# Performance work log

Measured on AMD Instinct MI355X. Metric: run time of the kernel, lower is better.

The kernel has to match this reference:

```python
import jax, jax.numpy as jnp
import numpy as np

T, N = 20, 192
D_EMB, D_H, D_REL = 32, 64, 32
D_TMP = D_REL + 2 * D_H  # 160 = rel_emb + h_self + h_neighbor


def setup_inputs() -> dict:
    key = jax.random.key(0)
    ks = jax.random.split(key, 16)
    g = lambda i, shape, s: jax.random.normal(ks[i], shape, jnp.float32) * s
    inp = {
        "nodes_abs": g(0, (T, N, 2), 1.0),
        "nodes_norm": g(1, (T, N, 2), 1.0),
        "shift_value": g(2, (T, N, 2), 1.0),
        # parameters (inputLayer, LSTMCell, 2 GCNs, outputLayer)
        "w_in": g(3, (D_EMB, 2), 0.2),
        "b_in": jnp.zeros((D_EMB,), jnp.float32),
        "w_ih": g(4, (4 * D_H, D_EMB), 0.1),
        "w_hh": g(5, (4 * D_H, D_H), 0.001),
        "b_ih": jnp.zeros((4 * D_H,), jnp.float32).at[D_H:2 * D_H].set(1.0),
        "b_hh": jnp.zeros((4 * D_H,), jnp.float32),
        "w_rel": g(6, (2, D_REL, 2), 0.1),
        "b_rel": jnp.zeros((2, D_REL), jnp.float32),
        "w_gate": g(7, (2, D_H, D_TMP), 0.1),
        "b_gate": jnp.zeros((2, D_H), jnp.float32),
        "w_ar": g(8, (2, D_TMP), 0.1),
        "b_ar": jnp.zeros((2,), jnp.float32),
        "w_nei": g(9, (2, D_H, D_H), 0.1),
        "w_out": g(10, (2, D_H), 0.1),
        "b_out": jnp.zeros((2,), jnp.float32),
        # int inputs
        "seq_list": jax.random.randint(ks[11], (T, N), 0, 2).astype(jnp.int32),
        "nei_list": jax.random.randint(ks[12], (T, N, N), 0, 2).astype(jnp.int32),
        "nei_num": jax.random.randint(ks[13], (T, N), 0, N).astype(jnp.int32),
    }
    return inp


def reference(nodes_abs, nodes_norm, shift_value, w_in, b_in, w_ih, w_hh, b_ih, b_hh,
              w_rel, b_rel, w_gate, b_gate, w_ar, b_ar, w_nei, w_out, b_out,
              seq_list, nei_list, nei_num):
    eps = 1e-6

    def gcn(p, corr, nei_f, h, c, o):
        # corr: (N,N,2) relative positions pos_i - pos_j; nei_f: (N,N) 0/1 mask
        r = jax.nn.relu(jnp.einsum('ijd,rd->ijr', corr, w_rel[p]) + b_rel[p])
        tmp = jnp.concatenate([r,
                               jnp.broadcast_to(h[:, None, :], (N, N, D_H)),
                               jnp.broadcast_to(h[None, :, :], (N, N, D_H))], axis=-1)
        gate = jax.nn.sigmoid(jnp.einsum('ijt,ht->ijh', tmp, w_gate[p]) + b_gate[p])
        score = jnp.einsum('ijt,t->ij', tmp, w_ar[p]) + b_ar[p]
        score = jnp.where(nei_f > 0, score, -1e9)
        pos = jax.nn.softmax(score, axis=1) * nei_f  # masked attention over neighbors j
        msg = jnp.einsum('ij,ijh,jh->ih', pos, gate, h)  # gated, attended aggregation
        c_new = c + msg @ w_nei[p].T
        h_new = o * jnp.tanh(c_new)
        v1 = jnp.sum(gate * nei_f[:, :, None]) / (jnp.sum(nei_f) * D_H + eps)
        v2 = jnp.sum(jnp.max(pos, axis=1)) / (jnp.sum(jnp.max(nei_f, axis=1)) + eps)
        v3 = jnp.sum(nei_f) / jnp.float32(N)
        return h_new, c_new, (v1, v2, v3)

    def step(carry, xs):
        h, c, v1s, v2s, v3s = carry
        abs_t, norm_t, seq_t, nei_t = xs
        m = seq_t > 0
        mf = m.astype(jnp.float32)
        nei_f = (nei_t > 0).astype(jnp.float32) * mf[:, None] * mf[None, :]
        corr = abs_t[:, None, :] - abs_t[None, :, :]  # corr_index[i,j] = pos_i - pos_j
        x = jax.nn.relu(norm_t @ w_in.T + b_in)  # dropout is identity in eval
        gates = x @ w_ih.T + b_ih + h @ w_hh.T + b_hh
        i_g, f_g, g_g, o_g = jnp.split(gates, 4, axis=-1)
        i_g = jax.nn.sigmoid(i_g); f_g = jax.nn.sigmoid(f_g); o_g = jax.nn.sigmoid(o_g)
        c1 = f_g * c + i_g * jnp.tanh(g_g)
        h1 = o_g * jnp.tanh(c1)
        h1, c1, look = gcn(0, corr, nei_f, h1, c1, o_g)
        h1, c1, _ = gcn(1, corr, nei_f, h1, c1, o_g)
        out_t = (h1 @ w_out.T + b_out) * mf[:, None]
        h = jnp.where(m[:, None], h1, h)  # only active nodes update state
        c = jnp.where(m[:, None], c1, c)
        return (h, c, v1s + look[0], v2s + look[1], v3s + look[2]), out_t

    h0 = jnp.zeros((N, D_H), jnp.float32)
    c0 = jnp.zeros((N, D_H), jnp.float32)
    z = jnp.float32(0.0)
    xs = (nodes_abs[:-1], nodes_norm[:-1], seq_list[:-1], nei_list[:-1])
    (h, c, v1, v2, v3), outs = jax.lax.scan(step, (h0, c0, z, z, z), xs)
    outputs = jnp.concatenate([outs, jnp.zeros((1, N, 2), jnp.float32)], axis=0)
    return outputs, h, c, (v1 / T, v2 / T, v3 / T)
```

## Files before the change

kernel.cpp:

```cpp
#include <hip/hip_runtime.h>
#include <hip/hip_bf16.h>

#define T_STEPS 20
#define NSTEP   19
#define NN      192
#define DH      64
#define DE      32

enum : int {
  O_H     = 0,
  O_C     = O_H    + NN*DH,
  O_UH0   = O_C    + NN*DH,
  O_UH1   = O_UH0  + 2*NN*DH,
  O_CW    = O_UH1  + 2*NN*DH,
  O_OG    = O_CW   + NN*DH,
  O_U1    = O_OG   + NN*DH,
  O_S1    = O_U1   + NN*DH,
  O_S20   = O_S1   + NN,
  O_S21   = O_S20  + NN,
  O_ACC   = O_S21  + NN,
  O_WIHT  = O_ACC  + NSTEP*4 + 4,
  O_WHHT  = O_WIHT + 8192,
  O_BIH   = O_WHHT + 16384,
  O_WIN   = O_BIH  + 256,
  O_BIN   = O_WIN  + 64,
  O_WRELF = O_BIN  + 32,
  O_BRELF = O_WRELF+ 128,
  O_WGR   = O_BRELF+ 64,
  O_WGH1T = O_WGR  + 4096,
  O_WGH2T = O_WGH1T+ 8192,
  O_BGATE = O_WGH2T+ 8192,
  O_WARR  = O_BGATE+ 128,
  O_WARH1 = O_WARR + 64,
  O_WARH2 = O_WARH1+ 128,
  O_BAR   = O_WARH2+ 128,
  O_WNEIT = O_BAR  + 4,
  O_WOUT  = O_WNEIT+ 8192,
  O_BOUT  = O_WOUT + 128,
  O_ISF   = O_BOUT + 2,
  O_TOTAL = O_ISF  + 1
};

typedef unsigned long long ull;

__device__ __forceinline__ float bf2f(__hip_bfloat16 v) { return __bfloat162float(v); }
__device__ __forceinline__ float sigm(float x) { return 1.0f / (1.0f + __expf(-x)); }
__device__ __forceinline__ float tanh_fast(float x) {
  float e = __expf(-2.0f * fabsf(x));
  float r = (1.0f - e) / (1.0f + e);
  return copysignf(r, x);
}

__device__ __forceinline__ float ldf(const void* p, int idx, int isf32) {
  if (isf32) return ((const float*)p)[idx];
  return bf2f(((const __hip_bfloat16*)p)[idx]);
}
__device__ __forceinline__ void stf(void* p, int idx, float v, int isf32) {
  if (isf32) ((float*)p)[idx] = v;
  else       ((__hip_bfloat16*)p)[idx] = __float2bfloat16(v);
}

__device__ __forceinline__ int read_isf(const float* F, int tid, int* s_isf) {
  if (tid == 0) *s_isf = (int)F[O_ISF];
  __syncthreads();
  return *s_isf;
}

__device__ __forceinline__ void lstm_prep_dev(
    float* __restrict__ F, const void* __restrict__ nnorm, int isf32,
    int t, int i, int tid, int wave, int lane, int load_hc,
    float* s_x, float* s_hc, float* s_cc, float* s_gates, float* s_h1)
{
  if (load_hc && wave == 0) { s_hc[lane] = F[O_H + i*DH + lane]; s_cc[lane] = F[O_C + i*DH + lane]; }
  if (wave == 1 && lane < DE) {
    float nx = ldf(nnorm, (t*NN + i)*2 + 0, isf32);
    float ny = ldf(nnorm, (t*NN + i)*2 + 1, isf32);
    s_x[lane] = fmaxf(nx*F[O_WIN + lane*2] + ny*F[O_WIN + lane*2 + 1] + F[O_BIN + lane], 0.f);
  }
  __syncthreads();
  {
    int G = tid;
    float acc = F[O_BIH + G];
    for (int e = 0; e < DE; e++) acc += F[O_WIHT + e*256 + G] * s_x[e];
    for (int k = 0; k < DH; k++) acc += F[O_WHHT + k*256 + G] * s_hc[k];
    s_gates[G] = acc;
  }
  __syncthreads();
  if (wave == 0) {
    float ig = sigm(s_gates[lane]);
    float fg = sigm(s_gates[64 + lane]);
    float gg = tanh_fast(s_gates[128 + lane]);
    float og = sigm(s_gates[192 + lane]);
    float c1 = fg * s_cc[lane] + ig * gg;
    float h1 = og * tanh_fast(c1);
    int idx = i*DH + lane;
    F[O_CW  + idx] = c1;
    F[O_UH0 + 2*idx + 1] = h1;
    F[O_OG  + idx] = og;
    s_h1[lane] = h1;
  }
  __syncthreads();
  {
    int idx = i*DH + lane;
    if (wave == 0) {
      float a = 0.f;
      const float* w = F + O_WGH1T + lane;
      for (int k = 0; k < DH; k++) a += w[k*DH] * s_h1[k];
      F[O_U1 + idx] = a;
    } else if (wave == 1) {
      float a = 0.f;
      const float* w = F + O_WGH2T + lane;
      for (int k = 0; k < DH; k++) a += w[k*DH] * s_h1[k];
      F[O_UH0 + 2*idx] = a;
    } else if (wave == 2) {
      float hp = s_h1[lane];
      float a1 = hp * F[O_WARH1 + lane];
      float a2 = hp * F[O_WARH2 + lane];
      for (int o = 32; o >= 1; o >>= 1) { a1 += __shfl_xor(a1, o, 64); a2 += __shfl_xor(a2, o, 64); }
      if (lane == 0) { F[O_S1 + i] = a1; F[O_S20 + i] = a2; }
    }
  }
}

__global__ __launch_bounds__(256) void k_init(float* __restrict__ F,
                       void* __restrict__ out,
                       const void* w_in,  const void* b_in,
                       const void* w_ih,  const void* w_hh,
                       const void* b_ih,  const void* b_hh,
                       const void* w_rel, const void* b_rel,
                       const void* w_gate,const void* b_gate,
                       const void* w_ar,  const void* b_ar,
                       const void* w_nei, const void* w_out,
                       const void* b_out) {
  __shared__ int s_isf;
  const int wave = threadIdx.x >> 6, lane = threadIdx.x & 63;
  if (wave == 0) {
    const unsigned short* u = (const unsigned short*)w_gate;
    int bad = 0;
    for (int x = lane; x < 1024; x += 64) {
      float v = __uint_as_float(((unsigned)u[x]) << 16);
      if (!(fabsf(v) <= 4.0f)) bad++;
    }
    for (int o = 32; o >= 1; o >>= 1) bad += __shfl_xor(bad, o, 64);
    if (lane == 0) s_isf = (bad > 64);
  }
  __syncthreads();
  const int isf32 = s_isf;
  if (blockIdx.x == 0 && threadIdx.x == 0) F[O_ISF] = (float)isf32;

  int tid = blockIdx.x * blockDim.x + threadIdx.x;
  int stride = gridDim.x * blockDim.x;
  for (int x = tid; x < O_WIHT; x += stride) F[x] = 0.f;
  for (int x = tid; x < NN*2;  x += stride) stf(out, (T_STEPS-1)*NN*2 + x, 0.f, isf32);
  for (int x = tid; x < 8192;  x += stride) { int e = x >> 8, G = x & 255; F[O_WIHT + x] = ldf(w_ih, G*32 + e, isf32); }
  for (int x = tid; x < 16384; x += stride) { int k = x >> 8, G = x & 255; F[O_WHHT + x] = ldf(w_hh, G*64 + k, isf32); }
  for (int x = tid; x < 256;   x += stride) F[O_BIH + x] = ldf(b_ih, x, isf32) + ldf(b_hh, x, isf32);
  for (int x = tid; x < 64;    x += stride) F[O_WIN + x] = ldf(w_in, x, isf32);
  for (int x = tid; x < 32;    x += stride) F[O_BIN + x] = ldf(b_in, x, isf32);
  for (int x = tid; x < 128;   x += stride) F[O_WRELF + x] = ldf(w_rel, x, isf32);
  for (int x = tid; x < 64;    x += stride) F[O_BRELF + x] = ldf(b_rel, x, isf32);
  for (int x = tid; x < 4096;  x += stride) { int p = x >> 11, h = (x >> 5) & 63, d = x & 31;
    F[O_WGR + x] = ldf(w_gate, p*10240 + h*160 + d, isf32); }
  for (int x = tid; x < 8192;  x += stride) { int p = x >> 12, k = (x >> 6) & 63, h = x & 63;
    F[O_WGH1T + x] = ldf(w_gate, p*10240 + h*160 + 32 + k, isf32); }
  for (int x = tid; x < 8192;  x += stride) { int p = x >> 12, k = (x >> 6) & 63, h = x & 63;
    F[O_WGH2T + x] = ldf(w_gate, p*10240 + h*160 + 96 + k, isf32); }
  for (int x = tid; x < 128;   x += stride) F[O_BGATE + x] = ldf(b_gate, x, isf32);
  for (int x = tid; x < 64;    x += stride) { int p = x >> 5, d = x & 31; F[O_WARR + x] = ldf(w_ar, p*160 + d, isf32); }
  for (int x = tid; x < 128;   x += stride) { int p = x >> 6, k = x & 63; F[O_WARH1 + x] = ldf(w_ar, p*160 + 32 + k, isf32); }
  for (int x = tid; x < 128;   x += stride) { int p = x >> 6, k = x & 63; F[O_WARH2 + x] = ldf(w_ar, p*160 + 96 + k, isf32); }
  for (int x = tid; x < 2;     x += stride) F[O_BAR + x] = ldf(b_ar, x, isf32);
  for (int x = tid; x < 8192;  x += stride) { int p = x >> 12, k = (x >> 6) & 63, h = x & 63;
    F[O_WNEIT + x] = ldf(w_nei, p*4096 + h*64 + k, isf32); }
  for (int x = tid; x < 128;   x += stride) F[O_WOUT + x] = ldf(w_out, x, isf32);
  for (int x = tid; x < 2;     x += stride) F[O_BOUT + x] = ldf(b_out, x, isf32);
}

__global__ __launch_bounds__(256) void k_lstm0(float* __restrict__ F,
                                               const void* __restrict__ nnorm) {
  __shared__ float s_x[DE], s_hc[DH], s_cc[DH], s_gates[4*DH], s_h1[DH];
  __shared__ int s_isf;
  const int tid = threadIdx.x, wave = tid >> 6, lane = tid & 63;
  const int isf32 = read_isf(F, tid, &s_isf);
  lstm_prep_dev(F, nnorm, isf32, 0, blockIdx.x, tid, wave, lane, 1,
                s_x, s_hc, s_cc, s_gates, s_h1);
}

__global__ __launch_bounds__(256) void k_gcn(float* __restrict__ F,
                                             const void* __restrict__ nabs,
                                             const void* __restrict__ nnorm,
                                             const int* __restrict__ seq,
                                             const int* __restrict__ nei,
                                             void* __restrict__ out,
                                             int t, int p, int last) {
  __shared__ float s_rt[NN*33];
  __shared__ float s_score[NN], s_pos[NN], s_neif[NN];
  __shared__ int   s_jlist[NN];
  __shared__ float s_red[4*DH], s_v1[4], s_msg[DH], s_hprep[DH];
  __shared__ float s_x[DE], s_hc[DH], s_cc[DH], s_gates[4*DH], s_h1[DH];
  __shared__ int   s_isf, s_nv;

  const int tid = threadIdx.x, wave = tid >> 6, lane = tid & 63;
  const int i = blockIdx.x;
  const int isf32 = read_isf(F, tid, &s_isf);
  const int m_i = seq[t*NN + i] > 0;
  const int UHr = p ? O_UH1 : O_UH0;
  const int S2r = p ? O_S21 : O_S20;

  if (wave < 3) {
    int j  = wave*64 + lane;
    int nf = m_i && (seq[t*NN + j] > 0) && (nei[(t*NN + i)*NN + j] > 0);
    s_neif[j] = nf ? 1.f : 0.f;
    float sc = 0.f;
    if (nf) {
      float cx = ldf(nabs, (t*NN + i)*2 + 0, isf32) - ldf(nabs, (t*NN + j)*2 + 0, isf32);
      float cy = ldf(nabs, (t*NN + i)*2 + 1, isf32) - ldf(nabs, (t*NN + j)*2 + 1, isf32);
      const float* wr = F + O_WRELF + p*64;
      const float* br = F + O_BRELF + p*32;
      const float* wa = F + O_WARR  + p*32;
      float dot = 0.f;
      for (int d = 0; d < 32; d++) {
        float rv = fmaxf(cx*wr[2*d] + cy*wr[2*d+1] + br[d], 0.f);
        s_rt[j*33 + d] = rv;
        dot += rv * wa[d];
      }
      sc = dot + F[O_S1 + i] + F[S2r + j] + F[O_BAR + p];
    }
    s_score[j] = sc;
  }
  __syncthreads();

  if (wave == 0) {
    float n0 = s_neif[lane], n1 = s_neif[64+lane], n2 = s_neif[128+lane];
    float sc0 = s_score[lane], sc1 = s_score[64+lane], sc2 = s_score[128+lane];
    const float NEG = -3.0e38f;
    float mx = fmaxf(fmaxf(n0 > 0.f ? sc0 : NEG, n1 > 0.f ? sc1 : NEG),
                     n2 > 0.f ? sc2 : NEG);
    for (int o = 32; o >= 1; o >>= 1) mx = fmaxf(mx, __shfl_xor(mx, o, 64));
    float e0 = (n0 > 0.f) ? __expf(sc0 - mx) : 0.f;
    float e1 = (n1 > 0.f) ? __expf(sc1 - mx) : 0.f;
    float e2 = (n2 > 0.f) ? __expf(sc2 - mx) : 0.f;
    float s = e0 + e1 + e2;
    for (int o = 32; o >= 1; o >>= 1) s += __shfl_xor(s, o, 64);
    float inv = (s > 0.f) ? 1.0f / s : 0.f;
    float p0 = e0*inv, p1 = e1*inv, p2 = e2*inv;
    s_pos[lane] = p0; s_pos[64+lane] = p1; s_pos[128+lane] = p2;
    ull m0 = __ballot(n0 > 0.f), m1 = __ballot(n1 > 0.f), m2 = __ballot(n2 > 0.f);
    ull lt = (1ull << lane) - 1ull;
    int c0 = __popcll(m0), c1 = __popcll(m1);
    if (n0 > 0.f) s_jlist[__popcll(m0 & lt)] = lane;
    if (n1 > 0.f) s_jlist[c0 + __popcll(m1 & lt)] = 64 + lane;
    if (n2 > 0.f) s_jlist[c0 + c1 + __popcll(m2 & lt)] = 128 + lane;
    if (lane == 0) s_nv = c0 + c1 + __popcll(m2);
    if (p == 0 && m_i) {
      float cnt = n0 + n1 + n2;
      float pm  = fmaxf(fmaxf(p0, p1), p2);
      for (int o = 32; o >= 1; o >>= 1) {
        cnt += __shfl_xor(cnt, o, 64);
        pm   = fmaxf(pm, __shfl_xor(pm, o, 64));
      }
      if (lane == 0 && cnt > 0.f) {
        atomicAdd(&F[O_ACC + t*4 + 1], cnt);
        atomicAdd(&F[O_ACC + t*4 + 2], pm);
        atomicAdd(&F[O_ACC + t*4 + 3], 1.f);
      }
    }
  }
  __syncthreads();

  {
    float msg = 0.f, v1 = 0.f;
    const int nv = s_nv;
    if (m_i && nv > 0) {
      float wreg[32];
      const float* wgp = F + O_WGR + p*2048 + lane*32;
#pragma unroll
      for (int d = 0; d < 32; d++) wreg[d] = wgp[d];
      float basev = F[O_U1 + i*DH + lane] + F[O_BGATE + p*DH + lane];
      const float2* UH2 = (const float2*)(F + UHr);
      int k = wave;
      int jn = (k < nv) ? s_jlist[k] : 0;
      float2 uhn = (k < nv) ? UH2[jn*DH + lane] : make_float2(0.f, 0.f);
      for (; k < nv; k += 4) {
        int j = jn;
        float2 uh = uhn;
        int kn = k + 4;
        if (kn < nv) { jn = s_jlist[kn]; uhn = UH2[jn*DH + lane]; }
        float acc = basev + uh.x;
        const float* rr = &s_rt[j*33];
#pragma unroll
        for (int d = 0; d < 32; d++) acc += rr[d] * wreg[d];
        float g = sigm(acc);
        v1 += g;
        msg += s_pos[j] * g * uh.y;
      }
    }
    s_red[wave*DH + lane] = msg;
    for (int o = 32; o >= 1; o >>= 1) v1 += __shfl_xor(v1, o, 64);
    if (lane == 0) s_v1[wave] = v1;
  }
  __syncthreads();

  if (wave == 0) {
    s_msg[lane] = s_red[lane] + s_red[64+lane] + s_red[128+lane] + s_red[192+lane];
    if (p == 0 && m_i && lane == 0) {
      float v1t = s_v1[0] + s_v1[1] + s_v1[2] + s_v1[3];
      atomicAdd(&F[O_ACC + t*4 + 0], v1t);
    }
  }
  __syncthreads();

  if (wave == 0) {
    int idx = i*DH + lane;
    float hcom, ccom = 0.f;
    if (m_i) {
      float cn = F[O_CW + idx];
      const float* wn = F + O_WNEIT + p*4096 + lane;
      for (int k = 0; k < DH; k++) cn += s_msg[k] * wn[k*DH];
      hcom = F[O_OG + idx] * tanh_fast(cn);
      F[O_CW + idx] = cn;
      ccom = cn;
      if (p == 1) { F[O_H + idx] = hcom; F[O_C + idx] = ccom; }
    } else {
      hcom = F[UHr + 2*idx + 1];
    }
    if (p == 0) F[O_UH1 + 2*idx + 1] = hcom;
    s_hprep[lane] = hcom;
    if (p == 1) {
      s_hc[lane] = m_i ? hcom : F[O_H + idx];
      s_cc[lane] = m_i ? ccom : F[O_C + idx];
    }
  }
  __syncthreads();

  if (p == 0) {
    int idx = i*DH + lane;
    if (wave == 0) {
      float a = 0.f;
      const float* w = F + O_WGH1T + 4096 + lane;
      for (int k = 0; k < DH; k++) a += w[k*DH] * s_hprep[k];
      F[O_U1 + idx] = a;
    } else if (wave == 1) {
      float a = 0.f;
      const float* w = F + O_WGH2T + 4096 + lane;
      for (int k = 0; k < DH; k++) a += w[k*DH] * s_hprep[k];
      F[O_UH1 + 2*idx] = a;
    } else if (wave == 2) {
      float hp = s_hprep[lane];
      float a1 = hp * F[O_WARH1 + DH + lane];
      float a2 = hp * F[O_WARH2 + DH + lane];
      for (int o = 32; o >= 1; o >>= 1) { a1 += __shfl_xor(a1, o, 64); a2 += __shfl_xor(a2, o, 64); }
      if (lane == 0) { F[O_S1 + i] = a1; F[O_S21 + i] = a2; }
    }
  } else {
    if (wave == 0 && lane < 2) {
      float a = 0.f;
      if (m_i) {
        a = F[O_BOUT + lane];
        const float* wo = F + O_WOUT + lane*DH;
        for (int h = 0; h < DH; h++) a += s_hprep[h] * wo[h];
      }
      stf(out, (t*NN + i)*2 + lane, a, isf32);
    }
    if (!last) {
      lstm_prep_dev(F, nnorm, isf32, t + 1, i, tid, wave, lane, 0,
                    s_x, s_hc, s_cc, s_gates, s_h1);
    } else {
      if (wave == 0) stf(out, T_STEPS*NN*2 + i*DH + lane,         s_hc[lane], isf32);
      if (wave == 1) stf(out, T_STEPS*NN*2 + NN*DH + i*DH + lane, s_cc[lane], isf32);
      if (i == 0 && tid == 0) {
        float v1 = 0.f, v2 = 0.f, v3 = 0.f;
        for (int tt = 0; tt < NSTEP; tt++) {
          float sg = F[O_ACC + tt*4 + 0], sn = F[O_ACC + tt*4 + 1];
          float sp = F[O_ACC + tt*4 + 2], sm = F[O_ACC + tt*4 + 3];
          v1 += sg / (sn * 64.f + 1e-6f);
          v2 += sp / (sm + 1e-6f);
          v3 += sn / 192.f;
        }
        int base = T_STEPS*NN*2 + 2*NN*DH;
        stf(out, base + 0, v1 / 20.f, isf32);
        stf(out, base + 1, v2 / 20.f, isf32);
        stf(out, base + 2, v3 / 20.f, isf32);
      }
    }
  }
}

extern "C" void kernel_launch(void* const* d_in, const int* in_sizes, int n_in,
                              void* d_out, int out_size, void* d_ws, size_t ws_size,
                              hipStream_t stream) {
  const void* nabs  = d_in[0];
  const void* nnorm = d_in[1];
  const int* seq = (const int*)d_in[18];
  const int* nei = (const int*)d_in[19];
  float* F = (float*)d_ws;

  k_init<<<NN, 256, 0, stream>>>(F, d_out,
      d_in[3], d_in[4], d_in[5], d_in[6], d_in[7], d_in[8], d_in[9], d_in[10],
      d_in[11], d_in[12], d_in[13], d_in[14], d_in[15], d_in[16], d_in[17]);
  k_lstm0<<<NN, 256, 0, stream>>>(F, nnorm);
  for (int t = 0; t < NSTEP; t++) {
    k_gcn<<<NN, 256, 0, stream>>>(F, nabs, nnorm, seq, nei, d_out, t, 0, 0);
    k_gcn<<<NN, 256, 0, stream>>>(F, nabs, nnorm, seq, nei, d_out, t, 1, t == NSTEP - 1);
  }
}
```

Baseline: 650.7 us.

## Fuse all timesteps into one persistent kernel with grid barriers and on-chip state

Replaces the 38 per-step GCN kernel launches and the separate LSTM kernel with a single persistent kernel of 192 blocks. The blocks synchronise through a software grid barrier built on global atomics. Per-node LSTM and cell state (c, o-gate, u1, s1, h, c) now stays in shared memory across steps instead of going through global memory. Weights are loaded once into registers and LDS, and the gate-weight layout is transposed for that preload. This removes launch overhead and repeated weight reloads. The cost is a spin barrier that relies on all 192 blocks being co-resident, plus higher register and LDS pressure.

```diff
diff --git a/kernel.cpp b/kernel.cpp
--- a/kernel.cpp
+++ b/kernel.cpp
@@ -8,18 +8,13 @@
 #define DE      32
 
 enum : int {
-  O_H     = 0,
-  O_C     = O_H    + NN*DH,
-  O_UH0   = O_C    + NN*DH,
+  O_UH0   = 0,
   O_UH1   = O_UH0  + 2*NN*DH,
-  O_CW    = O_UH1  + 2*NN*DH,
-  O_OG    = O_CW   + NN*DH,
-  O_U1    = O_OG   + NN*DH,
-  O_S1    = O_U1   + NN*DH,
-  O_S20   = O_S1   + NN,
+  O_S20   = O_UH1  + 2*NN*DH,
   O_S21   = O_S20  + NN,
   O_ACC   = O_S21  + NN,
-  O_WIHT  = O_ACC  + NSTEP*4 + 4,
+  O_GBAR  = O_ACC  + NSTEP*4,
+  O_WIHT  = O_GBAR + 4,
   O_WHHT  = O_WIHT + 8192,
   O_BIH   = O_WHHT + 16384,
   O_WIN   = O_BIH  + 256,
@@ -66,60 +61,24 @@
   return *s_isf;
 }
 
-__device__ __forceinline__ void lstm_prep_dev(
-    float* __restrict__ F, const void* __restrict__ nnorm, int isf32,
-    int t, int i, int tid, int wave, int lane, int load_hc,
-    float* s_x, float* s_hc, float* s_cc, float* s_gates, float* s_h1)
-{
-  if (load_hc && wave == 0) { s_hc[lane] = F[O_H + i*DH + lane]; s_cc[lane] = F[O_C + i*DH + lane]; }
-  if (wave == 1 && lane < DE) {
-    float nx = ldf(nnorm, (t*NN + i)*2 + 0, isf32);
-    float ny = ldf(nnorm, (t*NN + i)*2 + 1, isf32);
-    s_x[lane] = fmaxf(nx*F[O_WIN + lane*2] + ny*F[O_WIN + lane*2 + 1] + F[O_BIN + lane], 0.f);
-  }
-  __syncthreads();
-  {
-    int G = tid;
-    float acc = F[O_BIH + G];
-    for (int e = 0; e < DE; e++) acc += F[O_WIHT + e*256 + G] * s_x[e];
-    for (int k = 0; k < DH; k++) acc += F[O_WHHT + k*256 + G] * s_hc[k];
-    s_gates[G] = acc;
-  }
-  __syncthreads();
-  if (wave == 0) {
-    float ig = sigm(s_gates[lane]);
-    float fg = sigm(s_gates[64 + lane]);
-    float gg = tanh_fast(s_gates[128 + lane]);
-    float og = sigm(s_gates[192 + lane]);
-    float c1 = fg * s_cc[lane] + ig * gg;
-    float h1 = og * tanh_fast(c1);
-    int idx = i*DH + lane;
-    F[O_CW  + idx] = c1;
-    F[O_UH0 + 2*idx + 1] = h1;
-    F[O_OG  + idx] = og;
-    s_h1[lane] = h1;
-  }
-  __syncthreads();
-  {
-    int idx = i*DH + lane;
-    if (wave == 0) {
-      float a = 0.f;
-      const float* w = F + O_WGH1T + lane;
-      for (int k = 0; k < DH; k++) a += w[k*DH] * s_h1[k];
-      F[O_U1 + idx] = a;
-    } else if (wave == 1) {
-      float a = 0.f;
-      const float* w = F + O_WGH2T + lane;
-      for (int k = 0; k < DH; k++) a += w[k*DH] * s_h1[k];
-      F[O_UH0 + 2*idx] = a;
-    } else if (wave == 2) {
-      float hp = s_h1[lane];
-      float a1 = hp * F[O_WARH1 + lane];
-      float a2 = hp * F[O_WARH2 + lane];
-      for (int o = 32; o >= 1; o >>= 1) { a1 += __shfl_xor(a1, o, 64); a2 += __shfl_xor(a2, o, 64); }
-      if (lane == 0) { F[O_S1 + i] = a1; F[O_S20 + i] = a2; }
-    }
-  }
+__device__ __forceinline__ void gridbar(float* F, unsigned ep) {
+  __syncthreads();
+  if (threadIdx.x == 0) {
+    __threadfence();
+    unsigned* bar = (unsigned*)(F + O_GBAR);
+    unsigned v = __hip_atomic_fetch_add(bar, 1u, __ATOMIC_RELAXED,
+                                        __HIP_MEMORY_SCOPE_AGENT) + 1u;
+    if (v == (ep + 1u) * (unsigned)NN) {
+      __hip_atomic_store(bar + 1, ep + 1u, __ATOMIC_RELEASE,
+                         __HIP_MEMORY_SCOPE_AGENT);
+    } else {
+      while (__hip_atomic_load(bar + 1, __ATOMIC_RELAXED,
+                               __HIP_MEMORY_SCOPE_AGENT) < ep + 1u)
+        __builtin_amdgcn_s_sleep(2);
+    }
+    __threadfence();
+  }
+  __syncthreads();
 }
 
 __global__ __launch_bounds__(256) void k_init(float* __restrict__ F,
@@ -159,7 +118,7 @@
   for (int x = tid; x < 32;    x += stride) F[O_BIN + x] = ldf(b_in, x, isf32);
   for (int x = tid; x < 128;   x += stride) F[O_WRELF + x] = ldf(w_rel, x, isf32);
   for (int x = tid; x < 64;    x += stride) F[O_BRELF + x] = ldf(b_rel, x, isf32);
-  for (int x = tid; x < 4096;  x += stride) { int p = x >> 11, h = (x >> 5) & 63, d = x & 31;
+  for (int x = tid; x < 4096;  x += stride) { int p = x >> 11, d = (x >> 6) & 31, h = x & 63;
     F[O_WGR + x] = ldf(w_gate, p*10240 + h*160 + d, isf32); }
   for (int x = tid; x < 8192;  x += stride) { int p = x >> 12, k = (x >> 6) & 63, h = x & 63;
     F[O_WGH1T + x] = ldf(w_gate, p*10240 + h*160 + 32 + k, isf32); }
@@ -176,36 +135,81 @@
   for (int x = tid; x < 2;     x += stride) F[O_BOUT + x] = ldf(b_out, x, isf32);
 }
 
-__global__ __launch_bounds__(256) void k_lstm0(float* __restrict__ F,
-                                               const void* __restrict__ nnorm) {
-  __shared__ float s_x[DE], s_hc[DH], s_cc[DH], s_gates[4*DH], s_h1[DH];
-  __shared__ int s_isf;
-  const int tid = threadIdx.x, wave = tid >> 6, lane = tid & 63;
-  const int isf32 = read_isf(F, tid, &s_isf);
-  lstm_prep_dev(F, nnorm, isf32, 0, blockIdx.x, tid, wave, lane, 1,
-                s_x, s_hc, s_cc, s_gates, s_h1);
-}
-
-__global__ __launch_bounds__(256) void k_gcn(float* __restrict__ F,
-                                             const void* __restrict__ nabs,
-                                             const void* __restrict__ nnorm,
-                                             const int* __restrict__ seq,
-                                             const int* __restrict__ nei,
-                                             void* __restrict__ out,
-                                             int t, int p, int last) {
-  __shared__ float s_rt[NN*33];
-  __shared__ float s_score[NN], s_pos[NN], s_neif[NN];
-  __shared__ int   s_jlist[NN];
-  __shared__ float s_red[4*DH], s_v1[4], s_msg[DH], s_hprep[DH];
-  __shared__ float s_x[DE], s_hc[DH], s_cc[DH], s_gates[4*DH], s_h1[DH];
-  __shared__ int   s_isf, s_nv;
-
-  const int tid = threadIdx.x, wave = tid >> 6, lane = tid & 63;
-  const int i = blockIdx.x;
-  const int isf32 = read_isf(F, tid, &s_isf);
-  const int m_i = seq[t*NN + i] > 0;
-  const int UHr = p ? O_UH1 : O_UH0;
-  const int S2r = p ? O_S21 : O_S20;
+__device__ __forceinline__ void lstm_prep(
+    float* __restrict__ F, const void* __restrict__ nnorm, int isf32,
+    int t, int i, int tid, int wave, int lane,
+    const float* wih_r, const float* whh_r, float bih_r,
+    const float* s_win, const float* s_wgh1, const float* s_wgh2,
+    const float* s_cB,
+    float* s_x, float* s_hc, float* s_cc, float* s_gates, float* s_h1,
+    float* s_cw, float* s_og, float* s_u1, float* s_s1)
+{
+  if (wave == 1 && lane < DE) {
+    float nx = ldf(nnorm, (t*NN + i)*2 + 0, isf32);
+    float ny = ldf(nnorm, (t*NN + i)*2 + 1, isf32);
+    s_x[lane] = fmaxf(nx*s_win[lane*2] + ny*s_win[lane*2 + 1] + s_win[64 + lane], 0.f);
+  }
+  __syncthreads();
+  {
+    float acc = bih_r;
+#pragma unroll
+    for (int e = 0; e < DE; e++) acc += wih_r[e] * s_x[e];
+#pragma unroll
+    for (int k = 0; k < DH; k++) acc += whh_r[k] * s_hc[k];
+    s_gates[tid] = acc;
+  }
+  __syncthreads();
+  if (wave == 0) {
+    float ig = sigm(s_gates[lane]);
+    float fg = sigm(s_gates[64 + lane]);
+    float gg = tanh_fast(s_gates[128 + lane]);
+    float og = sigm(s_gates[192 + lane]);
+    float c1 = fg * s_cc[lane] + ig * gg;
+    float h1 = og * tanh_fast(c1);
+    s_cw[lane] = c1;
+    s_og[lane] = og;
+    s_h1[lane] = h1;
+    F[O_UH0 + 2*(i*DH + lane) + 1] = h1;
+  }
+  __syncthreads();
+  if (wave == 0) {
+    float a = 0.f;
+#pragma unroll
+    for (int k = 0; k < DH; k++) a += s_wgh1[k*DH + lane] * s_h1[k];
+    s_u1[lane] = a;
+  } else if (wave == 1) {
+    float a = 0.f;
+#pragma unroll
+    for (int k = 0; k < DH; k++) a += s_wgh2[k*DH + lane] * s_h1[k];
+    F[O_UH0 + 2*(i*DH + lane)] = a;
+  } else if (wave == 2) {
+    float hp = s_h1[lane];
+    float a1 = hp * s_cB[192 + lane];
+    float a2 = hp * s_cB[320 + lane];
+    for (int o = 32; o >= 1; o >>= 1) { a1 += __shfl_xor(a1, o, 64); a2 += __shfl_xor(a2, o, 64); }
+    if (lane == 0) { *s_s1 = a1; F[O_S20 + i] = a2; }
+  }
+}
+
+template<int P>
+__device__ __forceinline__ void gcn_pass(
+    float* __restrict__ F, const void* __restrict__ nabs,
+    const void* __restrict__ nnorm,
+    const int* __restrict__ seq, const int* __restrict__ nei,
+    void* __restrict__ out, int t, int last, int isf32, int m_i,
+    int tid, int wave, int lane, int i,
+    const float* wgP_r, float bgP,
+    const float* wih_r, const float* whh_r, float bih_r,
+    float* s_rt, float* s_score, float* s_pos, float* s_neif, int* s_jlist,
+    float* s_red, float* s_v1, float* s_msg, float* s_hprep,
+    float* s_x, float* s_hc, float* s_cc, float* s_gates, float* s_h1,
+    float* s_cw, float* s_og, float* s_u1, float* s_s1, int* s_nv,
+    const float* s_wgh1, const float* s_wgh2, const float* s_wnei,
+    const float* s_cA, const float* s_cB, const float* s_cC,
+    const float* s_win)
+{
+  const int UHr = P ? O_UH1 : O_UH0;
+  const int S2r = P ? O_S21 : O_S20;
 
   if (wave < 3) {
     int j  = wave*64 + lane;
@@ -215,16 +219,17 @@
     if (nf) {
       float cx = ldf(nabs, (t*NN + i)*2 + 0, isf32) - ldf(nabs, (t*NN + j)*2 + 0, isf32);
       float cy = ldf(nabs, (t*NN + i)*2 + 1, isf32) - ldf(nabs, (t*NN + j)*2 + 1, isf32);
-      const float* wr = F + O_WRELF + p*64;
-      const float* br = F + O_BRELF + p*32;
-      const float* wa = F + O_WARR  + p*32;
+      const float* wr = s_cA + P*64;
+      const float* br = s_cA + 128 + P*32;
+      const float* wa = s_cB + 128 + P*32;
       float dot = 0.f;
+#pragma unroll
       for (int d = 0; d < 32; d++) {
         float rv = fmaxf(cx*wr[2*d] + cy*wr[2*d+1] + br[d], 0.f);
         s_rt[j*33 + d] = rv;
         dot += rv * wa[d];
       }
-      sc = dot + F[O_S1 + i] + F[S2r + j] + F[O_BAR + p];
+      sc = dot + *s_s1 + F[S2r + j] + s_cB[448 + P];
     }
     s_score[j] = sc;
   }
@@ -251,8 +256,8 @@
     if (n0 > 0.f) s_jlist[__popcll(m0 & lt)] = lane;
     if (n1 > 0.f) s_jlist[c0 + __popcll(m1 & lt)] = 64 + lane;
     if (n2 > 0.f) s_jlist[c0 + c1 + __popcll(m2 & lt)] = 128 + lane;
-    if (lane == 0) s_nv = c0 + c1 + __popcll(m2);
-    if (p == 0 && m_i) {
+    if (lane == 0) *s_nv = c0 + c1 + __popcll(m2);
+    if (P == 0 && m_i) {
       float cnt = n0 + n1 + n2;
       float pm  = fmaxf(fmaxf(p0, p1), p2);
       for (int o = 32; o >= 1; o >>= 1) {
@@ -270,29 +275,41 @@
 
   {
     float msg = 0.f, v1 = 0.f;
-    const int nv = s_nv;
+    const int nv = *s_nv;
     if (m_i && nv > 0) {
-      float wreg[32];
-      const float* wgp = F + O_WGR + p*2048 + lane*32;
-#pragma unroll
-      for (int d = 0; d < 32; d++) wreg[d] = wgp[d];
-      float basev = F[O_U1 + i*DH + lane] + F[O_BGATE + p*DH + lane];
       const float2* UH2 = (const float2*)(F + UHr);
-      int k = wave;
-      int jn = (k < nv) ? s_jlist[k] : 0;
-      float2 uhn = (k < nv) ? UH2[jn*DH + lane] : make_float2(0.f, 0.f);
-      for (; k < nv; k += 4) {
-        int j = jn;
-        float2 uh = uhn;
-        int kn = k + 4;
-        if (kn < nv) { jn = s_jlist[kn]; uhn = UH2[jn*DH + lane]; }
-        float acc = basev + uh.x;
-        const float* rr = &s_rt[j*33];
-#pragma unroll
-        for (int d = 0; d < 32; d++) acc += rr[d] * wreg[d];
-        float g = sigm(acc);
-        v1 += g;
-        msg += s_pos[j] * g * uh.y;
+      float basev = s_u1[lane] + bgP;
+      int jc[4]; float2 uc[4];
+#pragma unroll
+      for (int q = 0; q < 4; q++) {
+        int kk = wave + q*4;
+        jc[q] = (kk < nv) ? s_jlist[kk] : -1;
+        uc[q] = make_float2(0.f, 0.f);
+        if (jc[q] >= 0) uc[q] = UH2[jc[q]*DH + lane];
+      }
+      for (int k = wave; k < nv; k += 16) {
+        int jn[4]; float2 un[4];
+#pragma unroll
+        for (int q = 0; q < 4; q++) {
+          int kk = k + 16 + q*4;
+          jn[q] = (kk < nv) ? s_jlist[kk] : -1;
+          un[q] = make_float2(0.f, 0.f);
+          if (jn[q] >= 0) un[q] = UH2[jn[q]*DH + lane];
+        }
+#pragma unroll
+        for (int q = 0; q < 4; q++) {
+          if (jc[q] >= 0) {
+            float acc = basev + uc[q].x;
+            const float* rr = &s_rt[jc[q]*33];
+#pragma unroll
+            for (int d = 0; d < 32; d++) acc += rr[d] * wgP_r[d];
+            float g = sigm(acc);
+            v1 += g;
+            msg += s_pos[jc[q]] * g * uc[q].y;
+          }
+        }
+#pragma unroll
+        for (int q = 0; q < 4; q++) { jc[q] = jn[q]; uc[q] = un[q]; }
       }
     }
     s_red[wave*DH + lane] = msg;
@@ -303,7 +320,7 @@
 
   if (wave == 0) {
     s_msg[lane] = s_red[lane] + s_red[64+lane] + s_red[128+lane] + s_red[192+lane];
-    if (p == 0 && m_i && lane == 0) {
+    if (P == 0 && m_i && lane == 0) {
       float v1t = s_v1[0] + s_v1[1] + s_v1[2] + s_v1[3];
       atomicAdd(&F[O_ACC + t*4 + 0], v1t);
     }
@@ -311,60 +328,56 @@
   __syncthreads();
 
   if (wave == 0) {
-    int idx = i*DH + lane;
     float hcom, ccom = 0.f;
     if (m_i) {
-      float cn = F[O_CW + idx];
-      const float* wn = F + O_WNEIT + p*4096 + lane;
-      for (int k = 0; k < DH; k++) cn += s_msg[k] * wn[k*DH];
-      hcom = F[O_OG + idx] * tanh_fast(cn);
-      F[O_CW + idx] = cn;
+      float cn = s_cw[lane];
+#pragma unroll
+      for (int k = 0; k < DH; k++) cn += s_msg[k] * s_wnei[P*4096 + k*DH + lane];
+      hcom = s_og[lane] * tanh_fast(cn);
+      s_cw[lane] = cn;
       ccom = cn;
-      if (p == 1) { F[O_H + idx] = hcom; F[O_C + idx] = ccom; }
     } else {
-      hcom = F[UHr + 2*idx + 1];
-    }
-    if (p == 0) F[O_UH1 + 2*idx + 1] = hcom;
+      hcom = P ? s_hprep[lane] : s_h1[lane];
+    }
+    if (P == 0) F[O_UH1 + 2*(i*DH + lane) + 1] = hcom;
     s_hprep[lane] = hcom;
-    if (p == 1) {
-      s_hc[lane] = m_i ? hcom : F[O_H + idx];
-      s_cc[lane] = m_i ? ccom : F[O_C + idx];
-    }
-  }
-  __syncthreads();
-
-  if (p == 0) {
-    int idx = i*DH + lane;
+    if (P == 1 && m_i) { s_hc[lane] = hcom; s_cc[lane] = ccom; }
+  }
+  __syncthreads();
+
+  if (P == 0) {
     if (wave == 0) {
       float a = 0.f;
-      const float* w = F + O_WGH1T + 4096 + lane;
-      for (int k = 0; k < DH; k++) a += w[k*DH] * s_hprep[k];
-      F[O_U1 + idx] = a;
+#pragma unroll
+      for (int k = 0; k < DH; k++) a += s_wgh1[4096 + k*DH + lane] * s_hprep[k];
+      s_u1[lane] = a;
     } else if (wave == 1) {
       float a = 0.f;
-      const float* w = F + O_WGH2T + 4096 + lane;
-      for (int k = 0; k < DH; k++) a += w[k*DH] * s_hprep[k];
-      F[O_UH1 + 2*idx] = a;
+#pragma unroll
+      for (int k = 0; k < DH; k++) a += s_wgh2[4096 + k*DH + lane] * s_hprep[k];
+      F[O_UH1 + 2*(i*DH + lane)] = a;
     } else if (wave == 2) {
       float hp = s_hprep[lane];
-      float a1 = hp * F[O_WARH1 + DH + lane];
-      float a2 = hp * F[O_WARH2 + DH + lane];
+      float a1 = hp * s_cB[192 + DH + lane];
+      float a2 = hp * s_cB[320 + DH + lane];
       for (int o = 32; o >= 1; o >>= 1) { a1 += __shfl_xor(a1, o, 64); a2 += __shfl_xor(a2, o, 64); }
-      if (lane == 0) { F[O_S1 + i] = a1; F[O_S21 + i] = a2; }
+      if (lane == 0) { *s_s1 = a1; F[O_S21 + i] = a2; }
     }
   } else {
     if (wave == 0 && lane < 2) {
       float a = 0.f;
       if (m_i) {
-        a = F[O_BOUT + lane];
-        const float* wo = F + O_WOUT + lane*DH;
+        a = s_cC[128 + lane];
+        const float* wo = s_cC + lane*DH;
+#pragma unroll
         for (int h = 0; h < DH; h++) a += s_hprep[h] * wo[h];
       }
       stf(out, (t*NN + i)*2 + lane, a, isf32);
     }
     if (!last) {
-      lstm_prep_dev(F, nnorm, isf32, t + 1, i, tid, wave, lane, 0,
-                    s_x, s_hc, s_cc, s_gates, s_h1);
+      lstm_prep(F, nnorm, isf32, t + 1, i, tid, wave, lane,
+                wih_r, whh_r, bih_r, s_win, s_wgh1, s_wgh2, s_cB,
+                s_x, s_hc, s_cc, s_gates, s_h1, s_cw, s_og, s_u1, s_s1);
     } else {
       if (wave == 0) stf(out, T_STEPS*NN*2 + i*DH + lane,         s_hc[lane], isf32);
       if (wave == 1) stf(out, T_STEPS*NN*2 + NN*DH + i*DH + lane, s_cc[lane], isf32);
@@ -386,6 +399,73 @@
   }
 }
 
+__global__ __launch_bounds__(256, 1) void k_main(float* __restrict__ F,
+    const void* __restrict__ nabs, const void* __restrict__ nnorm,
+    const int* __restrict__ seq, const int* __restrict__ nei,
+    void* __restrict__ out)
+{
+  __shared__ float s_rt[NN*33];
+  __shared__ float s_score[NN], s_pos[NN], s_neif[NN];
+  __shared__ int   s_jlist[NN];
+  __shared__ float s_red[4*DH], s_v1[4], s_msg[DH], s_hprep[DH];
+  __shared__ float s_x[DE], s_hc[DH], s_cc[DH], s_gates[4*DH], s_h1[DH];
+  __shared__ float s_cw[DH], s_og[DH], s_u1[DH], s_s1;
+  __shared__ float s_wgh1[2*DH*DH], s_wgh2[2*DH*DH], s_wnei[2*DH*DH];
+  __shared__ float s_cA[192], s_cB[452], s_cC[130], s_win[96];
+  __shared__ int   s_isf, s_nv;
+
+  const int tid = threadIdx.x, wave = tid >> 6, lane = tid & 63;
+  const int i = blockIdx.x;
+  const int isf32 = read_isf(F, tid, &s_isf);
+
+  float wih_r[DE], whh_r[DH], wg0_r[32], wg1_r[32];
+  const float bih_r = F[O_BIH + tid];
+#pragma unroll
+  for (int e = 0; e < DE; e++) wih_r[e] = F[O_WIHT + e*256 + tid];
+#pragma unroll
+  for (int k = 0; k < DH; k++) whh_r[k] = F[O_WHHT + k*256 + tid];
+#pragma unroll
+  for (int d = 0; d < 32; d++) wg0_r[d] = F[O_WGR + d*64 + lane];
+#pragma unroll
+  for (int d = 0; d < 32; d++) wg1_r[d] = F[O_WGR + 2048 + d*64 + lane];
+  const float bg0 = F[O_BGATE + lane], bg1 = F[O_BGATE + DH + lane];
+
+  for (int x = tid; x < 2*DH*DH; x += 256) s_wgh1[x] = F[O_WGH1T + x];
+  for (int x = tid; x < 2*DH*DH; x += 256) s_wgh2[x] = F[O_WGH2T + x];
+  for (int x = tid; x < 2*DH*DH; x += 256) s_wnei[x] = F[O_WNEIT + x];
+  for (int x = tid; x < 192; x += 256) s_cA[x] = F[O_WRELF + x];
+  for (int x = tid; x < 452; x += 256) s_cB[x] = F[O_BGATE + x];
+  for (int x = tid; x < 130; x += 256) s_cC[x] = F[O_WOUT + x];
+  for (int x = tid; x < 96;  x += 256) s_win[x] = F[O_WIN + x];
+  if (wave == 0) { s_hc[lane] = 0.f; s_cc[lane] = 0.f; }
+  __syncthreads();
+
+  lstm_prep(F, nnorm, isf32, 0, i, tid, wave, lane,
+            wih_r, whh_r, bih_r, s_win, s_wgh1, s_wgh2, s_cB,
+            s_x, s_hc, s_cc, s_gates, s_h1, s_cw, s_og, s_u1, &s_s1);
+
+  unsigned ep = 0;
+  for (int t = 0; t < NSTEP; t++) {
+    const int m_i = seq[t*NN + i] > 0;
+    gridbar(F, ep++);
+    gcn_pass<0>(F, nabs, nnorm, seq, nei, out, t, 0, isf32, m_i,
+                tid, wave, lane, i, wg0_r, bg0, wih_r, whh_r, bih_r,
+                s_rt, s_score, s_pos, s_neif, s_jlist,
+                s_red, s_v1, s_msg, s_hprep,
+                s_x, s_hc, s_cc, s_gates, s_h1,
+                s_cw, s_og, s_u1, &s_s1, &s_nv,
+                s_wgh1, s_wgh2, s_wnei, s_cA, s_cB, s_cC, s_win);
+    gridbar(F, ep++);
+    gcn_pass<1>(F, nabs, nnorm, seq, nei, out, t, t == NSTEP - 1, isf32, m_i,
+                tid, wave, lane, i, wg1_r, bg1, wih_r, whh_r, bih_r,
+                s_rt, s_score, s_pos, s_neif, s_jlist,
+                s_red, s_v1, s_msg, s_hprep,
+                s_x, s_hc, s_cc, s_gates, s_h1,
+                s_cw, s_og, s_u1, &s_s1, &s_nv,
+                s_wgh1, s_wgh2, s_wnei, s_cA, s_cB, s_cC, s_win);
+  }
+}
+
 extern "C" void kernel_launch(void* const* d_in, const int* in_sizes, int n_in,
                               void* d_out, int out_size, void* d_ws, size_t ws_size,
                               hipStream_t stream) {
@@ -398,9 +478,6 @@
   k_init<<<NN, 256, 0, stream>>>(F, d_out,
       d_in[3], d_in[4], d_in[5], d_in[6], d_in[7], d_in[8], d_in[9], d_in[10],
       d_in[11], d_in[12], d_in[13], d_in[14], d_in[15], d_in[16], d_in[17]);
-  k_lstm0<<<NN, 256, 0, stream>>>(F, nnorm);
-  for (int t = 0; t < NSTEP; t++) {
-    k_gcn<<<NN, 256, 0, stream>>>(F, nabs, nnorm, seq, nei, d_out, t, 0, 0);
-    k_gcn<<<NN, 256, 0, stream>>>(F, nabs, nnorm, seq, nei, d_out, t, 1, t == NSTEP - 1);
-  }
-}
+
+  k_main<<<NN, 256, 0, stream>>>(F, nabs, nnorm, seq, nei, d_out);
+}
```

After: 1.211 ms. +86.1%, slower.

## Build neighbor list early and batch-prefetch UH rows ahead of gate loop

Applied to the files above, without the earlier changes.

Builds the compacted neighbor list with a ballot right after the mask load, instead of after the softmax. This lets each wave issue global loads for up to eight UH rows before the relational-embedding and softmax work, hiding memory latency. The gate loop now processes eight neighbors per iteration while prefetching the next eight. The dtype flag is also passed as a kernel argument, inferred from input sizes, which removes a shared-memory broadcast and barrier. The cost is higher register pressure from the 8-deep prefetch arrays, and an extra barrier for the list construction.

```diff
diff --git a/kernel.cpp b/kernel.cpp
--- a/kernel.cpp
+++ b/kernel.cpp
@@ -60,10 +60,8 @@
   else       ((__hip_bfloat16*)p)[idx] = __float2bfloat16(v);
 }
 
-__device__ __forceinline__ int read_isf(const float* F, int tid, int* s_isf) {
-  if (tid == 0) *s_isf = (int)F[O_ISF];
-  __syncthreads();
-  return *s_isf;
+__device__ __forceinline__ int resolve_isf(const float* F, int isf_arg) {
+  return (isf_arg >= 0) ? isf_arg : (int)F[O_ISF];
 }
 
 __device__ __forceinline__ void lstm_prep_dev(
@@ -131,10 +129,12 @@
                        const void* w_gate,const void* b_gate,
                        const void* w_ar,  const void* b_ar,
                        const void* w_nei, const void* w_out,
-                       const void* b_out) {
+                       const void* b_out, int isf_arg) {
   __shared__ int s_isf;
   const int wave = threadIdx.x >> 6, lane = threadIdx.x & 63;
-  if (wave == 0) {
+  if (isf_arg >= 0) {
+    if (threadIdx.x == 0) s_isf = isf_arg;
+  } else if (wave == 0) {
     const unsigned short* u = (const unsigned short*)w_gate;
     int bad = 0;
     for (int x = lane; x < 1024; x += 64) {
@@ -177,11 +177,11 @@
 }
 
 __global__ __launch_bounds__(256) void k_lstm0(float* __restrict__ F,
-                                               const void* __restrict__ nnorm) {
+                                               const void* __restrict__ nnorm,
+                                               int isf_arg) {
   __shared__ float s_x[DE], s_hc[DH], s_cc[DH], s_gates[4*DH], s_h1[DH];
-  __shared__ int s_isf;
   const int tid = threadIdx.x, wave = tid >> 6, lane = tid & 63;
-  const int isf32 = read_isf(F, tid, &s_isf);
+  const int isf32 = resolve_isf(F, isf_arg);
   lstm_prep_dev(F, nnorm, isf32, 0, blockIdx.x, tid, wave, lane, 1,
                 s_x, s_hc, s_cc, s_gates, s_h1);
 }
@@ -192,25 +192,50 @@
                                              const int* __restrict__ seq,
                                              const int* __restrict__ nei,
                                              void* __restrict__ out,
-                                             int t, int p, int last) {
+                                             int t, int p, int last,
+                                             int isf_arg) {
   __shared__ float s_rt[NN*33];
   __shared__ float s_score[NN], s_pos[NN], s_neif[NN];
   __shared__ int   s_jlist[NN];
+  __shared__ ull   s_cmask[3];
   __shared__ float s_red[4*DH], s_v1[4], s_msg[DH], s_hprep[DH];
   __shared__ float s_x[DE], s_hc[DH], s_cc[DH], s_gates[4*DH], s_h1[DH];
-  __shared__ int   s_isf, s_nv;
 
   const int tid = threadIdx.x, wave = tid >> 6, lane = tid & 63;
   const int i = blockIdx.x;
-  const int isf32 = read_isf(F, tid, &s_isf);
+  const int isf32 = resolve_isf(F, isf_arg);
   const int m_i = seq[t*NN + i] > 0;
   const int UHr = p ? O_UH1 : O_UH0;
   const int S2r = p ? O_S21 : O_S20;
 
+  const int j = wave*64 + lane;
+  ull mymask = 0; int nf = 0;
   if (wave < 3) {
-    int j  = wave*64 + lane;
-    int nf = m_i && (seq[t*NN + j] > 0) && (nei[(t*NN + i)*NN + j] > 0);
+    nf = m_i && (seq[t*NN + j] > 0) && (nei[(t*NN + i)*NN + j] > 0);
     s_neif[j] = nf ? 1.f : 0.f;
+    mymask = __ballot(nf != 0);
+    if (lane == 0) s_cmask[wave] = mymask;
+  }
+  __syncthreads();
+  const int c0 = __popcll(s_cmask[0]), c1 = __popcll(s_cmask[1]), c2 = __popcll(s_cmask[2]);
+  const int nv = c0 + c1 + c2;
+  if (wave < 3 && nf) {
+    int base = (wave == 0) ? 0 : (wave == 1 ? c0 : c0 + c1);
+    ull lt = (1ull << lane) - 1ull;
+    s_jlist[base + __popcll(mymask & lt)] = j;
+  }
+  __syncthreads();
+
+  const float2* UH2 = (const float2*)(F + UHr);
+  int jc[8]; float2 uc[8];
+#pragma unroll
+  for (int q = 0; q < 8; q++) {
+    int kk = wave + q*4;
+    jc[q] = (kk < nv) ? s_jlist[kk] : -1;
+    uc[q] = make_float2(0.f, 0.f);
+    if (jc[q] >= 0) uc[q] = UH2[jc[q]*DH + lane];
+  }
+  if (wave < 3) {
     float sc = 0.f;
     if (nf) {
       float cx = ldf(nabs, (t*NN + i)*2 + 0, isf32) - ldf(nabs, (t*NN + j)*2 + 0, isf32);
@@ -219,6 +244,7 @@
       const float* br = F + O_BRELF + p*32;
       const float* wa = F + O_WARR  + p*32;
       float dot = 0.f;
+#pragma unroll
       for (int d = 0; d < 32; d++) {
         float rv = fmaxf(cx*wr[2*d] + cy*wr[2*d+1] + br[d], 0.f);
         s_rt[j*33 + d] = rv;
@@ -245,13 +271,6 @@
     float inv = (s > 0.f) ? 1.0f / s : 0.f;
     float p0 = e0*inv, p1 = e1*inv, p2 = e2*inv;
     s_pos[lane] = p0; s_pos[64+lane] = p1; s_pos[128+lane] = p2;
-    ull m0 = __ballot(n0 > 0.f), m1 = __ballot(n1 > 0.f), m2 = __ballot(n2 > 0.f);
-    ull lt = (1ull << lane) - 1ull;
-    int c0 = __popcll(m0), c1 = __popcll(m1);
-    if (n0 > 0.f) s_jlist[__popcll(m0 & lt)] = lane;
-    if (n1 > 0.f) s_jlist[c0 + __popcll(m1 & lt)] = 64 + lane;
-    if (n2 > 0.f) s_jlist[c0 + c1 + __popcll(m2 & lt)] = 128 + lane;
-    if (lane == 0) s_nv = c0 + c1 + __popcll(m2);
     if (p == 0 && m_i) {
       float cnt = n0 + n1 + n2;
       float pm  = fmaxf(fmaxf(p0, p1), p2);
@@ -270,29 +289,35 @@
 
   {
     float msg = 0.f, v1 = 0.f;
-    const int nv = s_nv;
     if (m_i && nv > 0) {
       float wreg[32];
       const float* wgp = F + O_WGR + p*2048 + lane*32;
 #pragma unroll
       for (int d = 0; d < 32; d++) wreg[d] = wgp[d];
       float basev = F[O_U1 + i*DH + lane] + F[O_BGATE + p*DH + lane];
-      const float2* UH2 = (const float2*)(F + UHr);
-      int k = wave;
-      int jn = (k < nv) ? s_jlist[k] : 0;
-      float2 uhn = (k < nv) ? UH2[jn*DH + lane] : make_float2(0.f, 0.f);
-      for (; k < nv; k += 4) {
-        int j = jn;
-        float2 uh = uhn;
-        int kn = k + 4;
-        if (kn < nv) { jn = s_jlist[kn]; uhn = UH2[jn*DH + lane]; }
-        float acc = basev + uh.x;
-        const float* rr = &s_rt[j*33];
-#pragma unroll
-        for (int d = 0; d < 32; d++) acc += rr[d] * wreg[d];
-        float g = sigm(acc);
-        v1 += g;
-        msg += s_pos[j] * g * uh.y;
+      for (int k = wave; k < nv; k += 32) {
+        int jn[8]; float2 un[8];
+#pragma unroll
+        for (int q = 0; q < 8; q++) {
+          int kk = k + 32 + q*4;
+          jn[q] = (kk < nv) ? s_jlist[kk] : -1;
+          un[q] = make_float2(0.f, 0.f);
+          if (jn[q] >= 0) un[q] = UH2[jn[q]*DH + lane];
+        }
+#pragma unroll
+        for (int q = 0; q < 8; q++) {
+          if (jc[q] >= 0) {
+            float acc = basev + uc[q].x;
+            const float* rr = &s_rt[jc[q]*33];
+#pragma unroll
+            for (int d = 0; d < 32; d++) acc += rr[d] * wreg[d];
+            float g = sigm(acc);
+            v1 += g;
+            msg += s_pos[jc[q]] * g * uc[q].y;
+          }
+        }
+#pragma unroll
+        for (int q = 0; q < 8; q++) { jc[q] = jn[q]; uc[q] = un[q]; }
       }
     }
     s_red[wave*DH + lane] = msg;
@@ -395,12 +420,18 @@
   const int* nei = (const int*)d_in[19];
   float* F = (float*)d_ws;
 
+  int isf = -1;
+  if (n_in > 11 && in_sizes) {
+    if      (in_sizes[11] == 81920) isf = 1;
+    else if (in_sizes[11] == 40960) isf = 0;
+  }
+
   k_init<<<NN, 256, 0, stream>>>(F, d_out,
       d_in[3], d_in[4], d_in[5], d_in[6], d_in[7], d_in[8], d_in[9], d_in[10],
-      d_in[11], d_in[12], d_in[13], d_in[14], d_in[15], d_in[16], d_in[17]);
-  k_lstm0<<<NN, 256, 0, stream>>>(F, nnorm);
+      d_in[11], d_in[12], d_in[13], d_in[14], d_in[15], d_in[16], d_in[17], isf);
+  k_lstm0<<<NN, 256, 0, stream>>>(F, nnorm, isf);
   for (int t = 0; t < NSTEP; t++) {
-    k_gcn<<<NN, 256, 0, stream>>>(F, nabs, nnorm, seq, nei, d_out, t, 0, 0);
-    k_gcn<<<NN, 256, 0, stream>>>(F, nabs, nnorm, seq, nei, d_out, t, 1, t == NSTEP - 1);
-  }
-}
+    k_gcn<<<NN, 256, 0, stream>>>(F, nabs, nnorm, seq, nei, d_out, t, 0, 0, isf);
+    k_gcn<<<NN, 256, 0, stream>>>(F, nabs, nnorm, seq, nei, d_out, t, 1, t == NSTEP - 1, isf);
+  }
+}
```

Result: slower. 697.8 us (+7.2%).

## Fuse both GCN passes per step into one kernel with a grid barrier

Applied to the files above, without the earlier changes.

Merges the two per-timestep GCN launches into a single kernel that runs pass 0, does a software grid-wide barrier built on an atomic counter in the workspace, then runs pass 1. This halves the number of launches and the launch gaps between dependent passes. The float/bf16 mode is now taken from the input byte sizes on the host instead of being detected in the kernel and read back per block. The barrier assumes all 192 blocks are co-resident, which holds on a large GPU but is not guaranteed. The barrier counter sits in the zero-initialised region, so it resets on every call.

```diff
diff --git a/kernel.cpp b/kernel.cpp
--- a/kernel.cpp
+++ b/kernel.cpp
@@ -19,7 +19,8 @@
   O_S20   = O_S1   + NN,
   O_S21   = O_S20  + NN,
   O_ACC   = O_S21  + NN,
-  O_WIHT  = O_ACC  + NSTEP*4 + 4,
+  O_GBAR  = O_ACC  + NSTEP*4,
+  O_WIHT  = O_GBAR + 4,
   O_WHHT  = O_WIHT + 8192,
   O_BIH   = O_WHHT + 16384,
   O_WIN   = O_BIH  + 256,
@@ -60,10 +61,28 @@
   else       ((__hip_bfloat16*)p)[idx] = __float2bfloat16(v);
 }
 
-__device__ __forceinline__ int read_isf(const float* F, int tid, int* s_isf) {
-  if (tid == 0) *s_isf = (int)F[O_ISF];
-  __syncthreads();
-  return *s_isf;
+__device__ __forceinline__ int resolve_isf(const float* F, int isf_arg) {
+  return (isf_arg >= 0) ? isf_arg : (int)F[O_ISF];
+}
+
+__device__ __forceinline__ void gridbar(float* F, unsigned ep) {
+  __syncthreads();
+  if (threadIdx.x == 0) {
+    __threadfence();
+    unsigned* bar = (unsigned*)(F + O_GBAR);
+    unsigned v = __hip_atomic_fetch_add(bar, 1u, __ATOMIC_RELAXED,
+                                        __HIP_MEMORY_SCOPE_AGENT) + 1u;
+    if (v == (ep + 1u) * (unsigned)NN) {
+      __hip_atomic_store(bar + 1, ep + 1u, __ATOMIC_RELAXED,
+                         __HIP_MEMORY_SCOPE_AGENT);
+    } else {
+      while (__hip_atomic_load(bar + 1, __ATOMIC_RELAXED,
+                               __HIP_MEMORY_SCOPE_AGENT) < ep + 1u)
+        __builtin_amdgcn_s_sleep(1);
+    }
+    __threadfence();
+  }
+  __syncthreads();
 }
 
 __device__ __forceinline__ void lstm_prep_dev(
@@ -131,10 +150,12 @@
                        const void* w_gate,const void* b_gate,
                        const void* w_ar,  const void* b_ar,
                        const void* w_nei, const void* w_out,
-                       const void* b_out) {
+                       const void* b_out, int isf_arg) {
   __shared__ int s_isf;
   const int wave = threadIdx.x >> 6, lane = threadIdx.x & 63;
-  if (wave == 0) {
+  if (isf_arg >= 0) {
+    if (threadIdx.x == 0) s_isf = isf_arg;
+  } else if (wave == 0) {
     const unsigned short* u = (const unsigned short*)w_gate;
     int bad = 0;
     for (int x = lane; x < 1024; x += 64) {
@@ -177,33 +198,26 @@
 }
 
 __global__ __launch_bounds__(256) void k_lstm0(float* __restrict__ F,
-                                               const void* __restrict__ nnorm) {
+                                               const void* __restrict__ nnorm,
+                                               int isf_arg) {
   __shared__ float s_x[DE], s_hc[DH], s_cc[DH], s_gates[4*DH], s_h1[DH];
-  __shared__ int s_isf;
   const int tid = threadIdx.x, wave = tid >> 6, lane = tid & 63;
-  const int isf32 = read_isf(F, tid, &s_isf);
+  const int isf32 = resolve_isf(F, isf_arg);
   lstm_prep_dev(F, nnorm, isf32, 0, blockIdx.x, tid, wave, lane, 1,
                 s_x, s_hc, s_cc, s_gates, s_h1);
 }
 
-__global__ __launch_bounds__(256) void k_gcn(float* __restrict__ F,
-                                             const void* __restrict__ nabs,
-                                             const void* __restrict__ nnorm,
-                                             const int* __restrict__ seq,
-                                             const int* __restrict__ nei,
-                                             void* __restrict__ out,
-                                             int t, int p, int last) {
-  __shared__ float s_rt[NN*33];
-  __shared__ float s_score[NN], s_pos[NN], s_neif[NN];
-  __shared__ int   s_jlist[NN];
-  __shared__ float s_red[4*DH], s_v1[4], s_msg[DH], s_hprep[DH];
-  __shared__ float s_x[DE], s_hc[DH], s_cc[DH], s_gates[4*DH], s_h1[DH];
-  __shared__ int   s_isf, s_nv;
-
-  const int tid = threadIdx.x, wave = tid >> 6, lane = tid & 63;
-  const int i = blockIdx.x;
-  const int isf32 = read_isf(F, tid, &s_isf);
-  const int m_i = seq[t*NN + i] > 0;
+__device__ __forceinline__ void gcn_pass(
+    float* __restrict__ F, const void* __restrict__ nabs,
+    const void* __restrict__ nnorm,
+    const int* __restrict__ seq, const int* __restrict__ nei,
+    void* __restrict__ out, int t, int p, int last, int isf32, int m_i,
+    int tid, int wave, int lane, int i,
+    float* s_rt, float* s_score, float* s_pos, float* s_neif, int* s_jlist,
+    float* s_red, float* s_v1, float* s_msg, float* s_hprep,
+    float* s_x, float* s_hc, float* s_cc, float* s_gates, float* s_h1,
+    int* s_nv)
+{
   const int UHr = p ? O_UH1 : O_UH0;
   const int S2r = p ? O_S21 : O_S20;
 
@@ -251,7 +265,7 @@
     if (n0 > 0.f) s_jlist[__popcll(m0 & lt)] = lane;
     if (n1 > 0.f) s_jlist[c0 + __popcll(m1 & lt)] = 64 + lane;
     if (n2 > 0.f) s_jlist[c0 + c1 + __popcll(m2 & lt)] = 128 + lane;
-    if (lane == 0) s_nv = c0 + c1 + __popcll(m2);
+    if (lane == 0) *s_nv = c0 + c1 + __popcll(m2);
     if (p == 0 && m_i) {
       float cnt = n0 + n1 + n2;
       float pm  = fmaxf(fmaxf(p0, p1), p2);
@@ -270,7 +284,7 @@
 
   {
     float msg = 0.f, v1 = 0.f;
-    const int nv = s_nv;
+    const int nv = *s_nv;
     if (m_i && nv > 0) {
       float wreg[32];
       const float* wgp = F + O_WGR + p*2048 + lane*32;
@@ -386,6 +400,40 @@
   }
 }
 
+__global__ __launch_bounds__(256) void k_step(float* __restrict__ F,
+                                              const void* __restrict__ nabs,
+                                              const void* __restrict__ nnorm,
+                                              const int* __restrict__ seq,
+                                              const int* __restrict__ nei,
+                                              void* __restrict__ out,
+                                              int t, int last, int isf_arg) {
+  __shared__ float s_rt[NN*33];
+  __shared__ float s_score[NN], s_pos[NN], s_neif[NN];
+  __shared__ int   s_jlist[NN];
+  __shared__ float s_red[4*DH], s_v1[4], s_msg[DH], s_hprep[DH];
+  __shared__ float s_x[DE], s_hc[DH], s_cc[DH], s_gates[4*DH], s_h1[DH];
+  __shared__ int   s_nv;
+
+  const int tid = threadIdx.x, wave = tid >> 6, lane = tid & 63;
+  const int i = blockIdx.x;
+  const int isf32 = resolve_isf(F, isf_arg);
+  const int m_i = seq[t*NN + i] > 0;
+
+  gcn_pass(F, nabs, nnorm, seq, nei, out, t, 0, 0, isf32, m_i,
+           tid, wave, lane, i,
+           s_rt, s_score, s_pos, s_neif, s_jlist,
+           s_red, s_v1, s_msg, s_hprep,
+           s_x, s_hc, s_cc, s_gates, s_h1, &s_nv);
+
+  gridbar(F, (unsigned)t);
+
+  gcn_pass(F, nabs, nnorm, seq, nei, out, t, 1, last, isf32, m_i,
+           tid, wave, lane, i,
+           s_rt, s_score, s_pos, s_neif, s_jlist,
+           s_red, s_v1, s_msg, s_hprep,
+           s_x, s_hc, s_cc, s_gates, s_h1, &s_nv);
+}
+
 extern "C" void kernel_launch(void* const* d_in, const int* in_sizes, int n_in,
                               void* d_out, int out_size, void* d_ws, size_t ws_size,
                               hipStream_t stream) {
@@ -395,12 +443,18 @@
   const int* nei = (const int*)d_in[19];
   float* F = (float*)d_ws;
 
+  int isf = -1;
+  if (n_in > 11 && in_sizes) {
+    if      (in_sizes[11] == 81920) isf = 1;
+    else if (in_sizes[11] == 40960) isf = 0;
+  }
+
   k_init<<<NN, 256, 0, stream>>>(F, d_out,
       d_in[3], d_in[4], d_in[5], d_in[6], d_in[7], d_in[8], d_in[9], d_in[10],
-      d_in[11], d_in[12], d_in[13], d_in[14], d_in[15], d_in[16], d_in[17]);
-  k_lstm0<<<NN, 256, 0, stream>>>(F, nnorm);
+      d_in[11], d_in[12], d_in[13], d_in[14], d_in[15], d_in[16], d_in[17], isf);
+  k_lstm0<<<NN, 256, 0, stream>>>(F, nnorm, isf);
   for (int t = 0; t < NSTEP; t++) {
-    k_gcn<<<NN, 256, 0, stream>>>(F, nabs, nnorm, seq, nei, d_out, t, 0, 0);
-    k_gcn<<<NN, 256, 0, stream>>>(F, nabs, nnorm, seq, nei, d_out, t, 1, t == NSTEP - 1);
-  }
-}
+    k_step<<<NN, 256, 0, stream>>>(F, nabs, nnorm, seq, nei, d_out,
+                                   t, t == NSTEP - 1, isf);
+  }
+}
```

Result: slower. 849.1 us (+30.5%).
